# Kernel optimization log

Hardware: AMD Instinct MI355X
Metric: run time of the kernel (lower is better)

The kernel has to match this reference:

```python
import jax, jax.numpy as jnp
import numpy as np

EMBED_DIM = 512
NUM_HEADS = 8
HEAD_DIM = EMBED_DIM // NUM_HEADS
LOCAL_SIZE = 17
NUM_WTOK = 64
SCALING = float(HEAD_DIM) ** -0.5


def get_overlap_segments(x, window_size):
    # x: (BH, T, D) -> (BH, T, W, D); centered zero-padded sliding windows
    if window_size % 2 == 0:
        window_size += 1
    pad = (window_size - 1) // 2
    xp = jnp.pad(x, ((0, 0), (pad, pad), (0, 0)))
    idx = jnp.arange(x.shape[1])[:, None] + jnp.arange(window_size)[None, :]
    return xp[:, idx, :]


def setup_inputs() -> dict:
    key = jax.random.key(0)
    k = jax.random.split(key, 5)
    B, T, E = 2, NUM_WTOK + 4096, EMBED_DIM
    s = 1.0 / np.sqrt(E).astype(np.float32)
    return {
        "x": jax.random.normal(k[0], (B, T, E), jnp.float32),
        "W_qkv": jax.random.normal(k[1], (E, 3 * E), jnp.float32) * s,
        "b_qkv": jax.random.normal(k[2], (3 * E,), jnp.float32) * 0.01,
        "W_out": jax.random.normal(k[3], (E, E), jnp.float32) * s,
        "b_out": jax.random.normal(k[4], (E,), jnp.float32) * 0.01,
    }


def reference(x, W_qkv, b_qkv, W_out, b_out):
    b, t, E = x.shape
    H, Dh, NW = NUM_HEADS, HEAD_DIM, NUM_WTOK
    BH = b * H
    qkv = x @ W_qkv + b_qkv
    Q, K, V = jnp.split(qkv, 3, axis=-1)
    Q = Q * SCALING

    def heads(z):  # (b,t,E) -> (b*H, t, Dh)
        return z.reshape(b, t, H, Dh).transpose(0, 2, 1, 3).reshape(BH, t, Dh)

    Q, K, V = heads(Q), heads(K), heads(V)
    Qw, Qf = Q[:, :NW], Q[:, NW:]
    Kw, Kf = K[:, :NW], K[:, NW:]
    Vw, Vf = V[:, :NW], V[:, NW:]
    t_fea = t - NW
    pad_len = (NW - t_fea % NW) % NW
    Kp = jnp.pad(Kf, ((0, 0), (0, pad_len), (0, 0)))
    Vp = jnp.pad(Vf, ((0, 0), (0, pad_len), (0, 0)))
    chunk = (t_fea + pad_len) // NW
    Kp = Kp.reshape(BH, NW, chunk, Dh)
    Vp = Vp.reshape(BH, NW, chunk, Dh)

    # ---- word-token stream: each wtok attends to its own key + its feature chunk
    Kcat = jnp.concatenate([Kw[:, :, None, :], Kp], axis=2)  # (BH, NW, 1+chunk, Dh)
    Vcat = jnp.concatenate([Vw[:, :, None, :], Vp], axis=2)
    aw = jax.nn.softmax(jnp.einsum('bnd,bncd->bnc', Qw, Kcat), axis=-1)
    out_wtok = jnp.einsum('bnc,bncd->bnd', aw, Vcat)  # (BH, NW, Dh)

    # broadcast each wtok output over its chunk of feature positions
    out_wtok_expa = jnp.repeat(out_wtok, chunk, axis=1)[:, :t_fea]  # (BH, t_fea, Dh)

    # ---- feature stream: local windowed attention + global wtok token
    Kseg = get_overlap_segments(Kf, LOCAL_SIZE)  # (BH, t_fea, W, Dh)
    Vseg = get_overlap_segments(Vf, LOCAL_SIZE)
    Kfull = jnp.concatenate([out_wtok_expa[:, :, None, :], Kseg], axis=2)
    scores = jnp.einsum('btd,btwd->btw', Qf, Kfull)  # (BH, t_fea, 1+W)

    w_wtok = scores[:, :, 0]  # (BH, t_fea)
    w_wtok = jnp.pad(w_wtok, ((0, 0), (0, pad_len)), constant_values=-jnp.inf)
    w_wtok = jax.nn.softmax(w_wtok.reshape(BH, NW, chunk), axis=-1)
    w_wtok = w_wtok.reshape(BH, NW * chunk)[:, :t_fea, None]
    w_fea = jax.nn.softmax(scores[:, :, 1:], axis=-1)
    attn = jnp.concatenate([w_wtok, w_fea], axis=-1)  # (BH, t_fea, 1+W)

    Vfull = jnp.concatenate([out_wtok_expa[:, :, None, :], Vseg], axis=2)
    out_fea = jnp.einsum('btw,btwd->btd', attn, Vfull)  # (BH, t_fea, Dh)

    out = jnp.concatenate([out_wtok, out_fea], axis=1)  # (BH, t, Dh)
    out = out.reshape(b, H, t, Dh).transpose(0, 2, 1, 3).reshape(b, t, E)
    return out @ W_out + b_out
```

## Files before the change

### kernel.cpp

```cpp
#include <hip/hip_runtime.h>
#include <hip/hip_bf16.h>
#include <math.h>

#define T_TOT 4160
#define H_N   8
#define NWTOK 64
#define TFEA  4096

typedef __bf16 bf16x8 __attribute__((ext_vector_type(8)));
typedef float  f32x4  __attribute__((ext_vector_type(4)));

__device__ inline ushort f2b(float f) {
  __hip_bfloat16 h = __float2bfloat16(f);
  return *reinterpret_cast<ushort*>(&h);
}
__device__ inline float b2f(ushort u) {
  union { uint i; float v; } a;
  a.i = ((uint)u) << 16;
  return a.v;
}
__device__ inline uint pk2(float a, float b) {
  return (uint)f2b(a) | ((uint)f2b(b) << 16);
}
__device__ inline void unpack8(uint4 u, float* f) {
  union { uint i; float v; } a;
  a.i = u.x << 16;        f[0] = a.v;
  a.i = u.x & 0xffff0000u; f[1] = a.v;
  a.i = u.y << 16;        f[2] = a.v;
  a.i = u.y & 0xffff0000u; f[3] = a.v;
  a.i = u.z << 16;        f[4] = a.v;
  a.i = u.z & 0xffff0000u; f[5] = a.v;
  a.i = u.w << 16;        f[6] = a.v;
  a.i = u.w & 0xffff0000u; f[7] = a.v;
}

__global__ __launch_bounds__(256) void conv_x(
    const float* __restrict__ X, ushort* __restrict__ Xb, int n8) {
  const int i = blockIdx.x * 256 + threadIdx.x;
  if (i >= n8) return;
  const float4 a = reinterpret_cast<const float4*>(X)[i * 2];
  const float4 b = reinterpret_cast<const float4*>(X)[i * 2 + 1];
  union { ushort u[8]; uint4 v; } r;
  r.u[0] = f2b(a.x); r.u[1] = f2b(a.y); r.u[2] = f2b(a.z); r.u[3] = f2b(a.w);
  r.u[4] = f2b(b.x); r.u[5] = f2b(b.y); r.u[6] = f2b(b.z); r.u[7] = f2b(b.w);
  reinterpret_cast<uint4*>(Xb)[i] = r.v;
}

__global__ __launch_bounds__(256) void conv_wT(
    const float* __restrict__ W, ushort* __restrict__ WT, int R, int C) {
  __shared__ float tile[64][65];
  const int r0 = blockIdx.x * 64, c0 = blockIdx.y * 64;
  const int tid = threadIdx.x;
  const int rr = tid >> 4, c4 = (tid & 15) * 4;
#pragma unroll
  for (int q = 0; q < 4; ++q) {
    const int r = q * 16 + rr;
    const float4 v = *reinterpret_cast<const float4*>(&W[(size_t)(r0 + r) * C + c0 + c4]);
    tile[r][c4] = v.x; tile[r][c4 + 1] = v.y; tile[r][c4 + 2] = v.z; tile[r][c4 + 3] = v.w;
  }
  __syncthreads();
#pragma unroll
  for (int q = 0; q < 4; ++q) {
    const int cr = q * 16 + rr;
    ushort4 o;
    o.x = f2b(tile[c4][cr]);
    o.y = f2b(tile[c4 + 1][cr]);
    o.z = f2b(tile[c4 + 2][cr]);
    o.w = f2b(tile[c4 + 3][cr]);
    *reinterpret_cast<ushort4*>(&WT[(size_t)(c0 + cr) * R + r0 + c4]) = o;
  }
}

template<int MODE>
__global__ __launch_bounds__(256) void gemm_mfma(
    const ushort* __restrict__ A, const ushort* __restrict__ BT,
    const float* __restrict__ bias, void* __restrict__ O0v,
    void* __restrict__ O1v, void* __restrict__ O2v) {
  __shared__ ushort sA[128 * 64];
  __shared__ ushort sB[128 * 64];
  const int tid = threadIdx.x;
  const int lane = tid & 63, wave = tid >> 6;
  const int m0 = blockIdx.x * 128, n0 = blockIdx.y * 128;
  const int wm = wave >> 1, wn = wave & 1;

  f32x4 acc[4][4] = {};

  auto stage = [&](int kt) {
    const ushort* Ag = A + (size_t)m0 * 512 + kt * 64;
    const ushort* Bg = BT + (size_t)n0 * 512 + kt * 64;
#pragma unroll
    for (int r = 0; r < 4; ++r) {
      const int rowbase = r * 32 + wave * 8;
      const int row = rowbase + (lane >> 3);
      const int c = lane & 7;
      const int cc = c ^ (row & 7);
      __builtin_amdgcn_global_load_lds(
          (const __attribute__((address_space(1))) void*)(Ag + (size_t)row * 512 + cc * 8),
          (__attribute__((address_space(3))) void*)(sA + rowbase * 64), 16, 0, 0);
      __builtin_amdgcn_global_load_lds(
          (const __attribute__((address_space(1))) void*)(Bg + (size_t)row * 512 + cc * 8),
          (__attribute__((address_space(3))) void*)(sB + rowbase * 64), 16, 0, 0);
    }
  };

  stage(0);
  for (int kt = 0; kt < 8; ++kt) {
    __syncthreads();
#pragma unroll
    for (int ks = 0; ks < 2; ++ks) {
      bf16x8 af[4], bfr[4];
      const int cc = ks * 4 + (lane >> 4);
      const int rA = wm * 64 + (lane & 15);
      const int rB = wn * 64 + (lane & 15);
#pragma unroll
      for (int i = 0; i < 4; ++i) {
        const int ra = rA + i * 16;
        af[i] = *reinterpret_cast<const bf16x8*>(&sA[ra * 64 + ((cc ^ (ra & 7)) << 3)]);
        const int rb = rB + i * 16;
        bfr[i] = *reinterpret_cast<const bf16x8*>(&sB[rb * 64 + ((cc ^ (rb & 7)) << 3)]);
      }
#pragma unroll
      for (int i = 0; i < 4; ++i)
#pragma unroll
        for (int j = 0; j < 4; ++j)
          acc[i][j] = __builtin_amdgcn_mfma_f32_16x16x32_bf16(af[i], bfr[j], acc[i][j], 0, 0, 0);
    }
    __syncthreads();
    if (kt < 7) stage(kt + 1);
  }

#pragma unroll
  for (int i = 0; i < 4; ++i) {
#pragma unroll
    for (int j = 0; j < 4; ++j) {
      const f32x4 a = acc[i][j];
      const int n = n0 + wn * 64 + j * 16 + (lane & 15);
      const float bv = bias[n];
#pragma unroll
      for (int r = 0; r < 4; ++r) {
        const int m = m0 + wm * 64 + i * 16 + ((lane >> 4) << 2) + r;
        const float v = a[r] + bv;
        if (MODE == 0) {
          const int bb = m / T_TOT, t = m - bb * T_TOT;
          const int which = n >> 9, e = n & 511;
          const int h = e >> 6, d = e & 63;
          const size_t idx = ((size_t)(bb * H_N + h) * T_TOT + t) * 64 + d;
          if (which == 0)      ((ushort*)O0v)[idx] = f2b(v * 0.125f);
          else if (which == 1) ((ushort*)O1v)[idx] = f2b(v);
          else                 ((ushort*)O2v)[idx] = f2b(v);
        } else {
          ((float*)O0v)[(size_t)m * 512 + n] = v;
        }
      }
    }
  }
}

__global__ __launch_bounds__(64) void wtok_attn(
    const ushort* __restrict__ Qb, const ushort* __restrict__ Kb,
    const ushort* __restrict__ Vb,
    float* __restrict__ OW, ushort* __restrict__ AObf) {
  const int bh = blockIdx.x >> 6;
  const int n = blockIdx.x & 63;
  const int lane = threadIdx.x;
  __shared__ float q[64];
  __shared__ float sc[65];
  __shared__ float aw[65];
  const size_t base = (size_t)bh * T_TOT * 64;
  q[lane] = b2f(Qb[base + n * 64 + lane]);
  __syncthreads();
  for (int c = lane; c < 65; c += 64) {
    const ushort* krow = (c == 0) ? &Kb[base + n * 64]
                                  : &Kb[base + (size_t)(NWTOK + n * 64 + (c - 1)) * 64];
    float acc = 0.f;
#pragma unroll
    for (int d0 = 0; d0 < 8; ++d0) {
      const uint4 u4 = *reinterpret_cast<const uint4*>(&krow[d0 * 8]);
      float f[8]; unpack8(u4, f);
#pragma unroll
      for (int k = 0; k < 8; ++k) acc += q[d0 * 8 + k] * f[k];
    }
    sc[c] = acc;
  }
  __syncthreads();
  const float v = sc[lane];
  float mx = fmaxf(v, sc[64]);
#pragma unroll
  for (int off = 32; off >= 1; off >>= 1) mx = fmaxf(mx, __shfl_xor(mx, off));
  const float e = __expf(v - mx);
  const float e64 = __expf(sc[64] - mx);
  float sum = e + (lane == 0 ? e64 : 0.f);
#pragma unroll
  for (int off = 32; off >= 1; off >>= 1) sum += __shfl_xor(sum, off);
  const float inv = 1.f / sum;
  aw[lane] = e * inv;
  if (lane == 0) aw[64] = e64 * inv;
  __syncthreads();
  float o = 0.f;
  for (int c = 0; c < 65; ++c) {
    const ushort* vrow = (c == 0) ? &Vb[base + n * 64]
                                  : &Vb[base + (size_t)(NWTOK + n * 64 + (c - 1)) * 64];
    o += aw[c] * b2f(vrow[lane]);
  }
  OW[(bh * 64 + n) * 64 + lane] = o;
  AObf[((size_t)(bh >> 3) * T_TOT + n) * 512 + (bh & 7) * 64 + lane] = f2b(o);
}

__global__ __launch_bounds__(256) void fea_attn(
    const ushort* __restrict__ Qb, const ushort* __restrict__ Kb,
    const ushort* __restrict__ Vb, const float* __restrict__ OW,
    ushort* __restrict__ AObf) {
  const int bh = blockIdx.x >> 6;
  const int n  = blockIdx.x & 63;
  const int tid = threadIdx.x;
  const int t  = tid & 63;
  const int wv = tid >> 6;
  __shared__ ushort Ks[80 * 64];
  __shared__ ushort Vs[80 * 64];
  __shared__ float ow[64];
  __shared__ float ps[4][18][64];
  const size_t base = (size_t)bh * T_TOT * 64;
  const int tok0 = n * 64;

#pragma unroll
  for (int it = 0; it < 3; ++it) {
    const int u = it * 256 + tid;
    if (u < 640) {
      const int r = u >> 3, c16 = u & 7;
      const int tok = tok0 - 8 + r;
      uint4 kv = make_uint4(0, 0, 0, 0), vv = make_uint4(0, 0, 0, 0);
      if (tok >= 0 && tok < TFEA) {
        kv = *reinterpret_cast<const uint4*>(&Kb[base + (size_t)(NWTOK + tok) * 64 + c16 * 8]);
        vv = *reinterpret_cast<const uint4*>(&Vb[base + (size_t)(NWTOK + tok) * 64 + c16 * 8]);
      }
      const int sw = (c16 ^ (r & 7)) << 3;
      *reinterpret_cast<uint4*>(&Ks[r * 64 + sw]) = kv;
      *reinterpret_cast<uint4*>(&Vs[r * 64 + sw]) = vv;
    }
  }
  if (tid < 64) ow[tid] = OW[(bh * 64 + n) * 64 + tid];

  float q[16];
  {
    const ushort* qr = &Qb[base + (size_t)(NWTOK + tok0 + t) * 64 + wv * 16];
#pragma unroll
    for (int h8 = 0; h8 < 2; ++h8) {
      const uint4 u4 = *reinterpret_cast<const uint4*>(&qr[h8 * 8]);
      unpack8(u4, &q[h8 * 8]);
    }
  }
  __syncthreads();

  const int d0a = wv * 2, d0b = wv * 2 + 1;
#pragma unroll
  for (int w = 0; w < 17; ++w) {
    const int r = t + w, rx = r & 7;
    float f[16];
    const uint4 ua = *reinterpret_cast<const uint4*>(&Ks[r * 64 + ((d0a ^ rx) << 3)]);
    const uint4 ub = *reinterpret_cast<const uint4*>(&Ks[r * 64 + ((d0b ^ rx) << 3)]);
    unpack8(ua, f); unpack8(ub, f + 8);
    float acc = 0.f;
#pragma unroll
    for (int k = 0; k < 16; ++k) acc += q[k] * f[k];
    ps[wv][w][t] = acc;
  }
  {
    float acc = 0.f;
#pragma unroll
    for (int k = 0; k < 16; ++k) acc += q[k] * ow[wv * 16 + k];
    ps[wv][17][t] = acc;
  }
  __syncthreads();

  float s[17];
#pragma unroll
  for (int w = 0; w < 17; ++w)
    s[w] = ps[0][w][t] + ps[1][w][t] + ps[2][w][t] + ps[3][w][t];
  float s0 = ps[0][17][t] + ps[1][17][t] + ps[2][17][t] + ps[3][17][t];

  float m = s[0];
#pragma unroll
  for (int w = 1; w < 17; ++w) m = fmaxf(m, s[w]);
  float sum = 0.f;
#pragma unroll
  for (int w = 0; w < 17; ++w) { s[w] = __expf(s[w] - m); sum += s[w]; }
  const float inv = 1.f / sum;
#pragma unroll
  for (int w = 0; w < 17; ++w) s[w] *= inv;

  float mx = s0;
#pragma unroll
  for (int off = 32; off >= 1; off >>= 1) mx = fmaxf(mx, __shfl_xor(mx, off));
  const float e0 = __expf(s0 - mx);
  float es = e0;
#pragma unroll
  for (int off = 32; off >= 1; off >>= 1) es += __shfl_xor(es, off);
  const float w0 = e0 / es;

  const int bb = bh >> 3, h = bh & 7;
  ushort* orow = &AObf[((size_t)bb * T_TOT + NWTOK + tok0 + t) * 512 + h * 64 + wv * 16];
#pragma unroll
  for (int hb = 0; hb < 2; ++hb) {
    const int d0 = wv * 2 + hb;
    float o[8];
#pragma unroll
    for (int k = 0; k < 8; ++k) o[k] = w0 * ow[d0 * 8 + k];
#pragma unroll
    for (int w = 0; w < 17; ++w) {
      const int r = t + w, rx = r & 7;
      const uint4 u4 = *reinterpret_cast<const uint4*>(&Vs[r * 64 + ((d0 ^ rx) << 3)]);
      float f[8]; unpack8(u4, f);
#pragma unroll
      for (int k = 0; k < 8; ++k) o[k] += s[w] * f[k];
    }
    uint4 st;
    st.x = pk2(o[0], o[1]); st.y = pk2(o[2], o[3]);
    st.z = pk2(o[4], o[5]); st.w = pk2(o[6], o[7]);
    *reinterpret_cast<uint4*>(&orow[hb * 8]) = st;
  }
}

extern "C" void kernel_launch(void* const* d_in, const int* in_sizes, int n_in,
                              void* d_out, int out_size, void* d_ws, size_t ws_size,
                              hipStream_t stream) {
  const float* x    = (const float*)d_in[0];
  const float* Wqkv = (const float*)d_in[1];
  const float* bqkv = (const float*)d_in[2];
  const float* Wout = (const float*)d_in[3];
  const float* bout = (const float*)d_in[4];
  float* out = (float*)d_out;

  const size_t SZ = (size_t)16 * T_TOT * 64;
  ushort* Qb = (ushort*)d_ws;
  ushort* Kb = Qb + SZ;
  ushort* Vb = Kb + SZ;
  float*  OW = (float*)(Vb + SZ);
  ushort* Xb    = (ushort*)(OW + 65536);
  ushort* WqkvT = Xb + SZ;
  ushort* WoutT = WqkvT + (size_t)1536 * 512;
  ushort* AObf  = WoutT + (size_t)512 * 512;

  conv_x<<<2080, 256, 0, stream>>>(x, Xb, (int)(SZ / 8));
  conv_wT<<<dim3(8, 24), 256, 0, stream>>>(Wqkv, WqkvT, 512, 1536);
  conv_wT<<<dim3(8, 8), 256, 0, stream>>>(Wout, WoutT, 512, 512);
  gemm_mfma<0><<<dim3(65, 12), 256, 0, stream>>>(Xb, WqkvT, bqkv, Qb, Kb, Vb);
  wtok_attn<<<1024, 64, 0, stream>>>(Qb, Kb, Vb, OW, AObf);
  fea_attn<<<1024, 256, 0, stream>>>(Qb, Kb, Vb, OW, AObf);
  gemm_mfma<1><<<dim3(65, 4), 256, 0, stream>>>(AObf, WoutT, bout, out, nullptr, nullptr);
}
```

Measured before the change: 143.2 us.

## Fuse word-token attention into feature attention kernel and merge weight conversions

The word-token attention is now computed inside the feature-attention block, which already stages the needed K/V chunk in shared memory. The wtok output goes to shared memory instead of a global OW buffer, removing one launch and the global round trip. The two weight transpose-conversions are also merged into one launch via a z grid dimension. Each block pays for an extra wave-wide softmax and 16-way shuffle reduction before its main work.

```diff
diff --git a/kernel.cpp b/kernel.cpp
--- a/kernel.cpp
+++ b/kernel.cpp
@@ -46,8 +46,14 @@
   reinterpret_cast<uint4*>(Xb)[i] = r.v;
 }
 
-__global__ __launch_bounds__(256) void conv_wT(
-    const float* __restrict__ W, ushort* __restrict__ WT, int R, int C) {
+__global__ __launch_bounds__(256) void conv_w2(
+    const float* __restrict__ W0, ushort* __restrict__ WT0,
+    const float* __restrict__ W1, ushort* __restrict__ WT1) {
+  const int z = blockIdx.z;
+  if (z == 1 && blockIdx.y >= 8) return;
+  const float* __restrict__ W = z ? W1 : W0;
+  ushort* __restrict__ WT = z ? WT1 : WT0;
+  const int C = z ? 512 : 1536;
   __shared__ float tile[64][65];
   const int r0 = blockIdx.x * 64, c0 = blockIdx.y * 64;
   const int tid = threadIdx.x;
@@ -67,7 +73,7 @@
     o.y = f2b(tile[c4 + 1][cr]);
     o.z = f2b(tile[c4 + 2][cr]);
     o.w = f2b(tile[c4 + 3][cr]);
-    *reinterpret_cast<ushort4*>(&WT[(size_t)(c0 + cr) * R + r0 + c4]) = o;
+    *reinterpret_cast<ushort4*>(&WT[(size_t)(c0 + cr) * 512 + r0 + c4]) = o;
   }
 }
 
@@ -156,60 +162,9 @@
   }
 }
 
-__global__ __launch_bounds__(64) void wtok_attn(
+__global__ __launch_bounds__(256) void fused_attn(
     const ushort* __restrict__ Qb, const ushort* __restrict__ Kb,
-    const ushort* __restrict__ Vb,
-    float* __restrict__ OW, ushort* __restrict__ AObf) {
-  const int bh = blockIdx.x >> 6;
-  const int n = blockIdx.x & 63;
-  const int lane = threadIdx.x;
-  __shared__ float q[64];
-  __shared__ float sc[65];
-  __shared__ float aw[65];
-  const size_t base = (size_t)bh * T_TOT * 64;
-  q[lane] = b2f(Qb[base + n * 64 + lane]);
-  __syncthreads();
-  for (int c = lane; c < 65; c += 64) {
-    const ushort* krow = (c == 0) ? &Kb[base + n * 64]
-                                  : &Kb[base + (size_t)(NWTOK + n * 64 + (c - 1)) * 64];
-    float acc = 0.f;
-#pragma unroll
-    for (int d0 = 0; d0 < 8; ++d0) {
-      const uint4 u4 = *reinterpret_cast<const uint4*>(&krow[d0 * 8]);
-      float f[8]; unpack8(u4, f);
-#pragma unroll
-      for (int k = 0; k < 8; ++k) acc += q[d0 * 8 + k] * f[k];
-    }
-    sc[c] = acc;
-  }
-  __syncthreads();
-  const float v = sc[lane];
-  float mx = fmaxf(v, sc[64]);
-#pragma unroll
-  for (int off = 32; off >= 1; off >>= 1) mx = fmaxf(mx, __shfl_xor(mx, off));
-  const float e = __expf(v - mx);
-  const float e64 = __expf(sc[64] - mx);
-  float sum = e + (lane == 0 ? e64 : 0.f);
-#pragma unroll
-  for (int off = 32; off >= 1; off >>= 1) sum += __shfl_xor(sum, off);
-  const float inv = 1.f / sum;
-  aw[lane] = e * inv;
-  if (lane == 0) aw[64] = e64 * inv;
-  __syncthreads();
-  float o = 0.f;
-  for (int c = 0; c < 65; ++c) {
-    const ushort* vrow = (c == 0) ? &Vb[base + n * 64]
-                                  : &Vb[base + (size_t)(NWTOK + n * 64 + (c - 1)) * 64];
-    o += aw[c] * b2f(vrow[lane]);
-  }
-  OW[(bh * 64 + n) * 64 + lane] = o;
-  AObf[((size_t)(bh >> 3) * T_TOT + n) * 512 + (bh & 7) * 64 + lane] = f2b(o);
-}
-
-__global__ __launch_bounds__(256) void fea_attn(
-    const ushort* __restrict__ Qb, const ushort* __restrict__ Kb,
-    const ushort* __restrict__ Vb, const float* __restrict__ OW,
-    ushort* __restrict__ AObf) {
+    const ushort* __restrict__ Vb, ushort* __restrict__ AObf) {
   const int bh = blockIdx.x >> 6;
   const int n  = blockIdx.x & 63;
   const int tid = threadIdx.x;
@@ -217,6 +172,9 @@
   const int wv = tid >> 6;
   __shared__ ushort Ks[80 * 64];
   __shared__ ushort Vs[80 * 64];
+  __shared__ ushort kwr[64];
+  __shared__ ushort vwr[64];
+  __shared__ float qw[64];
   __shared__ float ow[64];
   __shared__ float ps[4][18][64];
   const size_t base = (size_t)bh * T_TOT * 64;
@@ -238,7 +196,18 @@
       *reinterpret_cast<uint4*>(&Vs[r * 64 + sw]) = vv;
     }
   }
-  if (tid < 64) ow[tid] = OW[(bh * 64 + n) * 64 + tid];
+  if (tid < 8)
+    *reinterpret_cast<uint4*>(&kwr[tid * 8]) =
+        *reinterpret_cast<const uint4*>(&Kb[base + n * 64 + tid * 8]);
+  else if (tid < 16)
+    *reinterpret_cast<uint4*>(&vwr[(tid - 8) * 8]) =
+        *reinterpret_cast<const uint4*>(&Vb[base + n * 64 + (tid - 8) * 8]);
+  else if (tid < 32) {
+    const int j = tid - 16;
+    const ushort4 u = *reinterpret_cast<const ushort4*>(&Qb[base + n * 64 + j * 4]);
+    qw[j * 4 + 0] = b2f(u.x); qw[j * 4 + 1] = b2f(u.y);
+    qw[j * 4 + 2] = b2f(u.z); qw[j * 4 + 3] = b2f(u.w);
+  }
 
   float q[16];
   {
@@ -247,6 +216,67 @@
     for (int h8 = 0; h8 < 2; ++h8) {
       const uint4 u4 = *reinterpret_cast<const uint4*>(&qr[h8 * 8]);
       unpack8(u4, &q[h8 * 8]);
+    }
+  }
+  __syncthreads();
+
+  float aw_l, aw0;
+  {
+    const int row = t + 8, r7 = row & 7;
+    float acc = 0.f, acc0 = 0.f;
+#pragma unroll
+    for (int g = 0; g < 8; ++g) {
+      float f[8], f0[8];
+      const uint4 u  = *reinterpret_cast<const uint4*>(&Ks[row * 64 + ((g ^ r7) << 3)]);
+      const uint4 u0 = *reinterpret_cast<const uint4*>(&kwr[g * 8]);
+      unpack8(u, f); unpack8(u0, f0);
+#pragma unroll
+      for (int k = 0; k < 8; ++k) {
+        const float qv = qw[g * 8 + k];
+        acc  += qv * f[k];
+        acc0 += qv * f0[k];
+      }
+    }
+    float mx = fmaxf(acc, acc0);
+#pragma unroll
+    for (int off = 32; off >= 1; off >>= 1) mx = fmaxf(mx, __shfl_xor(mx, off));
+    const float e = __expf(acc - mx), e0 = __expf(acc0 - mx);
+    float sum = e;
+#pragma unroll
+    for (int off = 32; off >= 1; off >>= 1) sum += __shfl_xor(sum, off);
+    sum += e0;
+    aw_l = e / sum;
+    aw0  = e0 / sum;
+  }
+  {
+    float pv[16];
+    const int row = t + 8, r7 = row & 7;
+    const float a0 = (t == 0) ? aw0 : 0.f;
+#pragma unroll
+    for (int hb = 0; hb < 2; ++hb) {
+      const int g = wv * 2 + hb;
+      float f[8], f0[8];
+      const uint4 u  = *reinterpret_cast<const uint4*>(&Vs[row * 64 + ((g ^ r7) << 3)]);
+      const uint4 u0 = *reinterpret_cast<const uint4*>(&vwr[g * 8]);
+      unpack8(u, f); unpack8(u0, f0);
+#pragma unroll
+      for (int k = 0; k < 8; ++k) pv[hb * 8 + k] = aw_l * f[k] + a0 * f0[k];
+    }
+#pragma unroll
+    for (int off = 1; off < 64; off <<= 1)
+#pragma unroll
+      for (int k = 0; k < 16; ++k) pv[k] += __shfl_xor(pv[k], off);
+    if (t == 0) {
+#pragma unroll
+      for (int k = 0; k < 16; ++k) ow[wv * 16 + k] = pv[k];
+      uint4 s1, s2;
+      s1.x = pk2(pv[0], pv[1]);   s1.y = pk2(pv[2], pv[3]);
+      s1.z = pk2(pv[4], pv[5]);   s1.w = pk2(pv[6], pv[7]);
+      s2.x = pk2(pv[8], pv[9]);   s2.y = pk2(pv[10], pv[11]);
+      s2.z = pk2(pv[12], pv[13]); s2.w = pk2(pv[14], pv[15]);
+      ushort* orow = &AObf[((size_t)(bh >> 3) * T_TOT + n) * 512 + (bh & 7) * 64 + wv * 16];
+      *reinterpret_cast<uint4*>(&orow[0]) = s1;
+      *reinterpret_cast<uint4*>(&orow[8]) = s2;
     }
   }
   __syncthreads();
@@ -334,17 +364,14 @@
   ushort* Qb = (ushort*)d_ws;
   ushort* Kb = Qb + SZ;
   ushort* Vb = Kb + SZ;
-  float*  OW = (float*)(Vb + SZ);
-  ushort* Xb    = (ushort*)(OW + 65536);
+  ushort* Xb    = Vb + SZ;
   ushort* WqkvT = Xb + SZ;
   ushort* WoutT = WqkvT + (size_t)1536 * 512;
   ushort* AObf  = WoutT + (size_t)512 * 512;
 
   conv_x<<<2080, 256, 0, stream>>>(x, Xb, (int)(SZ / 8));
-  conv_wT<<<dim3(8, 24), 256, 0, stream>>>(Wqkv, WqkvT, 512, 1536);
-  conv_wT<<<dim3(8, 8), 256, 0, stream>>>(Wout, WoutT, 512, 512);
+  conv_w2<<<dim3(8, 24, 2), 256, 0, stream>>>(Wqkv, WqkvT, Wout, WoutT);
   gemm_mfma<0><<<dim3(65, 12), 256, 0, stream>>>(Xb, WqkvT, bqkv, Qb, Kb, Vb);
-  wtok_attn<<<1024, 64, 0, stream>>>(Qb, Kb, Vb, OW, AObf);
-  fea_attn<<<1024, 256, 0, stream>>>(Qb, Kb, Vb, OW, AObf);
+  fused_attn<<<1024, 256, 0, stream>>>(Qb, Kb, Vb, AObf);
   gemm_mfma<1><<<dim3(65, 4), 256, 0, stream>>>(AObf, WoutT, bout, out, nullptr, nullptr);
 }
```

Measured after the change: 142.9 us. Within noise of the previous version (-0.2%).
